# Optimization experiments

Measured on AMD Instinct MI355X. Metric: run time of the kernel, lower is better.

## Reference

```python
import jax, jax.numpy as jnp
import numpy as np

N_HEAD = 16
RMS_EPS = 1.1920928955078125e-07  # torch float32 finfo eps (F.rms_norm default)


def _apply_rotary(x, cos, sin):
    # x: [B,T,H,D], cos/sin: [1,T,1,D/2]
    d = x.shape[-1] // 2
    x1, x2 = x[..., :d], x[..., d:]
    return jnp.concatenate([x1 * cos + x2 * sin, -x1 * sin + x2 * cos], axis=-1)


def _rms_norm(x):
    var = jnp.mean(jnp.square(x), axis=-1, keepdims=True)
    return x * jax.lax.rsqrt(var + RMS_EPS)


def setup_inputs() -> dict:
    key = jax.random.key(0)
    ks = jax.random.split(key, 5)
    B, T, C, H = 2, 2048, 1024, N_HEAD
    D = C // H
    x = jax.random.normal(ks[0], (B, T, C), dtype=jnp.float32)
    cos = jax.random.uniform(ks[1], (1, T, 1, D // 2), dtype=jnp.float32)
    sin = jax.random.uniform(ks[2], (1, T, 1, D // 2), dtype=jnp.float32)
    kv_w = jax.random.normal(ks[3], (C, C), dtype=jnp.float32) * (C ** -0.5)
    proj_w = jax.random.normal(ks[4], (C, C), dtype=jnp.float32) * (C ** -0.5)
    return {"x": x, "cos": cos, "sin": sin, "kv_w": kv_w, "proj_w": proj_w, "window_left": 1024}


def reference(x, cos, sin, kv_w, proj_w, window_left):
    B, T, C = x.shape
    H = N_HEAD
    D = C // H
    scale = D ** -0.5

    q = x.reshape(B, T, H, D)                       # no Q projection
    kv = (x @ kv_w.T).reshape(B, T, H, D)           # tied K=V projection

    q = _rms_norm(_apply_rotary(q, cos, sin))
    kv = _rms_norm(_apply_rotary(kv, cos, sin))

    # scores: [B,H,T,T]
    scores = jnp.einsum('bqhd,bkhd->bhqk', q, kv) * scale

    pos = jnp.arange(T)
    dist = pos[:, None] - pos[None, :]              # query_pos - key_pos
    allowed = (dist >= 0) & (dist <= window_left)   # causal + sliding window
    scores = jnp.where(allowed[None, None], scores, -jnp.inf)

    attn = jax.nn.softmax(scores, axis=-1)
    out = jnp.einsum('bhqk,bkhd->bqhd', attn, kv).reshape(B, T, C)
    return out @ proj_w.T
```

## Files before the change

kernel.cpp:

```cpp
#include <hip/hip_runtime.h>
#include <hip/hip_bf16.h>

using u16 = unsigned short;
typedef __attribute__((ext_vector_type(8))) short short8v;
typedef __attribute__((ext_vector_type(4))) float f32x4;

#define MFMA16(a, b, c) __builtin_amdgcn_mfma_f32_16x16x32_bf16((a), (b), (c), 0, 0, 0)

#define GLOAD16(g, l) __builtin_amdgcn_global_load_lds(                       \
    (const __attribute__((address_space(1))) void*)(const void*)(g),          \
    (__attribute__((address_space(3))) void*)(void*)(l), 16, 0, 0)

static __device__ __forceinline__ u16 f2bf(float x) {
  __hip_bfloat16 h = __float2bfloat16(x);
  return __builtin_bit_cast(u16, h);
}

__global__ __launch_bounds__(256) void cast_f32_bf16(const float* __restrict__ s,
                                                     u16* __restrict__ d, int n) {
  int i = (blockIdx.x * 256 + threadIdx.x) * 4;
  if (i >= n) return;
  float4 v = *reinterpret_cast<const float4*>(s + i);
  ushort4 o;
  o.x = f2bf(v.x); o.y = f2bf(v.y); o.z = f2bf(v.z); o.w = f2bf(v.w);
  *reinterpret_cast<ushort4*>(d + i) = o;
}

__global__ __launch_bounds__(256) void gemm_bt(const u16* __restrict__ A,
                                               const u16* __restrict__ Bt,
                                               float* __restrict__ C,
                                               int M, int N, int K) {
  __shared__ u16 As[64 * 32];
  __shared__ u16 Bs[128 * 32];
  int bm = blockIdx.x, bn = blockIdx.y;
  int tid = threadIdx.x;
  int wid = tid >> 6, l = tid & 63, lr = l & 15, lg = l >> 4;
  int wr = wid >> 1, wc = wid & 1;

  int srow = l >> 2, scol = (l & 3) * 8;
  const u16* Ag  = A  + (size_t)(bm * 64 + wid * 16 + srow) * K + scol;
  const u16* Bg0 = Bt + (size_t)(bn * 128 + wid * 32 + srow) * K + scol;
  const u16* Bg1 = Bg0 + (size_t)16 * K;
  u16* Asb  = &As[wid * 512];
  u16* Bsb0 = &Bs[wid * 1024];
  u16* Bsb1 = &Bs[wid * 1024 + 512];

  f32x4 acc[2][4];
#pragma unroll
  for (int m = 0; m < 2; m++)
#pragma unroll
    for (int n = 0; n < 4; n++) acc[m][n] = (f32x4){0.f, 0.f, 0.f, 0.f};

  for (int k0 = 0; k0 < K; k0 += 32) {
    __syncthreads();
    GLOAD16(Ag + k0, Asb);
    GLOAD16(Bg0 + k0, Bsb0);
    GLOAD16(Bg1 + k0, Bsb1);
    __syncthreads();

    short8v af[2], bfr[4];
#pragma unroll
    for (int m = 0; m < 2; m++)
      af[m] = *reinterpret_cast<const short8v*>(&As[(wr * 32 + m * 16 + lr) * 32 + lg * 8]);
#pragma unroll
    for (int n = 0; n < 4; n++)
      bfr[n] = *reinterpret_cast<const short8v*>(&Bs[(wc * 64 + n * 16 + lr) * 32 + lg * 8]);
#pragma unroll
    for (int m = 0; m < 2; m++)
#pragma unroll
      for (int n = 0; n < 4; n++) acc[m][n] = MFMA16(af[m], bfr[n], acc[m][n]);
  }

#pragma unroll
  for (int m = 0; m < 2; m++)
#pragma unroll
    for (int n = 0; n < 4; n++)
#pragma unroll
      for (int r = 0; r < 4; r++) {
        int row = bm * 64 + wr * 32 + m * 16 + lg * 4 + r;
        int col = bn * 128 + wc * 64 + n * 16 + lr;
        C[(size_t)row * N + col] = acc[m][n][r];
      }
}

__global__ __launch_bounds__(256) void rope_rms(const float* __restrict__ src,
                                                u16* __restrict__ dst,
                                                const float* __restrict__ cosp,
                                                const float* __restrict__ sinp,
                                                float scale) {
  int R = blockIdx.x * 4 + (threadIdx.x >> 6);
  int l = threadIdx.x & 63;
  int h = R & 15;
  int bt = R >> 4;
  int t = bt & 2047, b = bt >> 11;

  float v = src[((size_t)R << 6) + l];
  float p = __shfl_xor(v, 32);
  float c = cosp[(t << 5) + (l & 31)];
  float s = sinp[(t << 5) + (l & 31)];
  float r = v * c + ((l < 32) ? p * s : -p * s);
  float sq = r * r;
  sq += __shfl_xor(sq, 32);
  sq += __shfl_xor(sq, 16);
  sq += __shfl_xor(sq, 8);
  sq += __shfl_xor(sq, 4);
  sq += __shfl_xor(sq, 2);
  sq += __shfl_xor(sq, 1);
  float inv = rsqrtf(sq * (1.0f / 64.0f) + 1.1920928955078125e-07f) * scale;
  dst[((((size_t)b * 16 + h) * 2048 + t) << 6) + l] = f2bf(r * inv);
}

__global__ __launch_bounds__(256) void transpose_td(const u16* __restrict__ src,
                                                    u16* __restrict__ dst) {
  __shared__ u16 Ld[64][72];
  int t0 = blockIdx.x << 6, bh = blockIdx.y;
  int tid = threadIdx.x;
#pragma unroll
  for (int i = 0; i < 2; i++) {
    int c = tid + i * 256, tr = c >> 3, sg = c & 7;
    *reinterpret_cast<short8v*>(&Ld[tr][sg * 8]) =
        *reinterpret_cast<const short8v*>(src + ((size_t)bh * 2048 + t0 + tr) * 64 + sg * 8);
  }
  __syncthreads();
#pragma unroll
  for (int i = 0; i < 2; i++) {
    int c = tid + i * 256, dr = c >> 3, sg = c & 7;
    short8v v;
#pragma unroll
    for (int j = 0; j < 8; j++) v[j] = (short)Ld[sg * 8 + j][dr];
    *reinterpret_cast<short8v*>(dst + ((size_t)bh * 64 + dr) * 2048 + t0 + sg * 8) = v;
  }
}

__global__ __launch_bounds__(256) void attn_swa(const u16* __restrict__ Q,
                                                const u16* __restrict__ KV,
                                                const u16* __restrict__ KVt,
                                                u16* __restrict__ O,
                                                const int* __restrict__ winp) {
  const int T = 2048;
  int bid = blockIdx.x;
  int bh = bid & 31;
  int qi = 31 - (bid >> 5);
  int q0 = qi << 6;
  int b = bh >> 4, h = bh & 15;
  int W = *winp;
  int tid = threadIdx.x;
  int wid = tid >> 6, l = tid & 63, lr = l & 15, lg = l >> 4;

  __shared__ u16 Kl[64][72];
  __shared__ u16 Vt[64][72];
  __shared__ u16 Pl[4][16][72];

  const u16* Qb = Q + (((size_t)bh * T + q0 + wid * 16 + lr) << 6);
  short8v aq0 = *reinterpret_cast<const short8v*>(Qb + lg * 8);
  short8v aq1 = *reinterpret_cast<const short8v*>(Qb + 32 + lg * 8);

  const short one_bf = (short)0x3F80;
  short8v vones = {one_bf, one_bf, one_bf, one_bf, one_bf, one_bf, one_bf, one_bf};

  float m_run[4], l_run[4];
  f32x4 oacc[4];
#pragma unroll
  for (int r = 0; r < 4; r++) { m_run[r] = -1e30f; l_run[r] = 0.f; }
#pragma unroll
  for (int dt = 0; dt < 4; dt++) oacc[dt] = (f32x4){0.f, 0.f, 0.f, 0.f};

  int lo = q0 - W;
  if (lo < 0) lo = 0;
  lo &= ~63;

  const u16* KVbh  = KV + (((size_t)bh * T) << 6);
  const u16* KVtbh = KVt + ((size_t)bh << 6) * T;
  int r8 = tid >> 3, sg = tid & 7;

  short8v vK0 = *reinterpret_cast<const short8v*>(KVbh + ((size_t)(lo + r8) << 6) + sg * 8);
  short8v vK1 = *reinterpret_cast<const short8v*>(KVbh + ((size_t)(lo + r8 + 32) << 6) + sg * 8);
  short8v vV0 = *reinterpret_cast<const short8v*>(KVtbh + (size_t)r8 * T + lo + sg * 8);
  short8v vV1 = *reinterpret_cast<const short8v*>(KVtbh + (size_t)(r8 + 32) * T + lo + sg * 8);

  for (int kt = lo; kt <= q0; kt += 64) {
    __syncthreads();
    *reinterpret_cast<short8v*>(&Kl[r8][sg * 8]) = vK0;
    *reinterpret_cast<short8v*>(&Kl[r8 + 32][sg * 8]) = vK1;
    *reinterpret_cast<short8v*>(&Vt[r8][sg * 8]) = vV0;
    *reinterpret_cast<short8v*>(&Vt[r8 + 32][sg * 8]) = vV1;
    __syncthreads();
    if (kt < q0) {
      vK0 = *reinterpret_cast<const short8v*>(KVbh + ((size_t)(kt + 64 + r8) << 6) + sg * 8);
      vK1 = *reinterpret_cast<const short8v*>(KVbh + ((size_t)(kt + 64 + r8 + 32) << 6) + sg * 8);
      vV0 = *reinterpret_cast<const short8v*>(KVtbh + (size_t)r8 * T + kt + 64 + sg * 8);
      vV1 = *reinterpret_cast<const short8v*>(KVtbh + (size_t)(r8 + 32) * T + kt + 64 + sg * 8);
    }

    f32x4 s[4];
#pragma unroll
    for (int nt = 0; nt < 4; nt++) {
      s[nt] = (f32x4){0.f, 0.f, 0.f, 0.f};
      short8v b0 = *reinterpret_cast<const short8v*>(&Kl[nt * 16 + lr][lg * 8]);
      s[nt] = MFMA16(aq0, b0, s[nt]);
      short8v b1 = *reinterpret_cast<const short8v*>(&Kl[nt * 16 + lr][32 + lg * 8]);
      s[nt] = MFMA16(aq1, b1, s[nt]);
    }

    bool edge = (kt + 63 > q0 + wid * 16) || ((q0 - kt) + wid * 16 + 15 > W);

    float al4[4];
#pragma unroll
    for (int r = 0; r < 4; r++) {
      float sv[4], mt;
      if (edge) {
        int t = q0 + wid * 16 + lg * 4 + r;
        mt = -3e38f;
#pragma unroll
        for (int nt = 0; nt < 4; nt++) {
          int k = kt + nt * 16 + lr;
          float val = ((k <= t) && (t - k <= W)) ? s[nt][r] : -3e38f;
          sv[nt] = val;
          mt = fmaxf(mt, val);
        }
      } else {
#pragma unroll
        for (int nt = 0; nt < 4; nt++) sv[nt] = s[nt][r];
        mt = fmaxf(fmaxf(sv[0], sv[1]), fmaxf(sv[2], sv[3]));
      }
      mt = fmaxf(mt, __shfl_xor(mt, 1));
      mt = fmaxf(mt, __shfl_xor(mt, 2));
      mt = fmaxf(mt, __shfl_xor(mt, 4));
      mt = fmaxf(mt, __shfl_xor(mt, 8));
      float mn = fmaxf(m_run[r], mt);
      float al = exp2f(m_run[r] - mn);
      m_run[r] = mn;
      al4[r] = al;
#pragma unroll
      for (int nt = 0; nt < 4; nt++) {
        Pl[wid][lg * 4 + r][nt * 16 + lr] = f2bf(exp2f(sv[nt] - mn));
      }
#pragma unroll
      for (int dt = 0; dt < 4; dt++) oacc[dt][r] *= al;
    }

    short8v ap0 = *reinterpret_cast<const short8v*>(&Pl[wid][lr][lg * 8]);
    short8v ap1 = *reinterpret_cast<const short8v*>(&Pl[wid][lr][32 + lg * 8]);
    f32x4 psum = (f32x4){0.f, 0.f, 0.f, 0.f};
    psum = MFMA16(ap0, vones, psum);
    psum = MFMA16(ap1, vones, psum);
#pragma unroll
    for (int dt = 0; dt < 4; dt++) {
      short8v v0 = *reinterpret_cast<const short8v*>(&Vt[dt * 16 + lr][lg * 8]);
      oacc[dt] = MFMA16(ap0, v0, oacc[dt]);
      short8v v1 = *reinterpret_cast<const short8v*>(&Vt[dt * 16 + lr][32 + lg * 8]);
      oacc[dt] = MFMA16(ap1, v1, oacc[dt]);
    }
#pragma unroll
    for (int r = 0; r < 4; r++) l_run[r] = l_run[r] * al4[r] + psum[r];
  }

#pragma unroll
  for (int r = 0; r < 4; r++) {
    int t = q0 + wid * 16 + lg * 4 + r;
    float inv = 1.f / l_run[r];
#pragma unroll
    for (int dt = 0; dt < 4; dt++) {
      O[(((size_t)b * T + t) << 10) + (h << 6) + dt * 16 + lr] = f2bf(oacc[dt][r] * inv);
    }
  }
}

extern "C" void kernel_launch(void* const* d_in, const int* in_sizes, int n_in,
                              void* d_out, int out_size, void* d_ws, size_t ws_size,
                              hipStream_t stream) {
  (void)in_sizes; (void)n_in; (void)out_size; (void)ws_size;
  const float* x    = (const float*)d_in[0];
  const float* cosp = (const float*)d_in[1];
  const float* sinp = (const float*)d_in[2];
  const float* kvw  = (const float*)d_in[3];
  const float* pw   = (const float*)d_in[4];
  const int*   win  = (const int*)d_in[5];

  char* w = (char*)d_ws;
  u16*   xbf   = (u16*)(w);
  u16*   kvwbf = (u16*)(w + (8u << 20));
  u16*   pwbf  = (u16*)(w + (10u << 20));
  float* kvf   = (float*)(w + (12u << 20));
  u16*   kvt   = (u16*)(w + (12u << 20));
  u16*   aout  = (u16*)(w + (20u << 20));
  u16*   kvbf  = (u16*)(w + (28u << 20));
  u16*   qbf   = xbf;

  cast_f32_bf16<<<4096, 256, 0, stream>>>(x, xbf, 4194304);
  cast_f32_bf16<<<1024, 256, 0, stream>>>(kvw, kvwbf, 1048576);
  cast_f32_bf16<<<1024, 256, 0, stream>>>(pw, pwbf, 1048576);

  gemm_bt<<<dim3(64, 8), 256, 0, stream>>>(xbf, kvwbf, kvf, 4096, 1024, 1024);

  rope_rms<<<16384, 256, 0, stream>>>(x, qbf, cosp, sinp, 0.18033688011112042f);
  rope_rms<<<16384, 256, 0, stream>>>(kvf, kvbf, cosp, sinp, 1.0f);

  transpose_td<<<dim3(32, 32), 256, 0, stream>>>(kvbf, kvt);

  attn_swa<<<1024, 256, 0, stream>>>(qbf, kvbf, kvt, aout, win);

  gemm_bt<<<dim3(64, 8), 256, 0, stream>>>(aout, pwbf, (float*)d_out, 4096, 1024, 1024);
}
```

Measured before the change: 203.9 us.

## Double-buffer GEMM LDS tiles and swizzle workgroup order

The bf16 GEMM now ping-pongs between two LDS buffers. It issues the global-to-LDS loads for the next K slice before running the MFMAs on the current one, and uses one barrier per iteration instead of two. It also remaps the block index with an XCD-style swizzle so neighbouring tiles share cache on the same die. The cost is doubled shared memory per block. Correctness also depends on the single barrier covering the async LDS load completion, which relies on an implicit vmcnt wait at the barrier.

New measurement: 199.5 us. -2.2%, faster.

```diff
diff --git a/kernel.cpp b/kernel.cpp
--- a/kernel.cpp
+++ b/kernel.cpp
@@ -30,9 +30,12 @@
                                                const u16* __restrict__ Bt,
                                                float* __restrict__ C,
                                                int M, int N, int K) {
-  __shared__ u16 As[64 * 32];
-  __shared__ u16 Bs[128 * 32];
-  int bm = blockIdx.x, bn = blockIdx.y;
+  __shared__ u16 As[2][64 * 32];
+  __shared__ u16 Bs[2][128 * 32];
+  unsigned flat = blockIdx.y * gridDim.x + blockIdx.x;
+  unsigned nwg = gridDim.x * gridDim.y;
+  unsigned swz = (flat & 7) * (nwg >> 3) + (flat >> 3);
+  int bm = swz % gridDim.x, bn = swz / gridDim.x;
   int tid = threadIdx.x;
   int wid = tid >> 6, l = tid & 63, lr = l & 15, lg = l >> 4;
   int wr = wid >> 1, wc = wid & 1;
@@ -41,9 +44,6 @@
   const u16* Ag  = A  + (size_t)(bm * 64 + wid * 16 + srow) * K + scol;
   const u16* Bg0 = Bt + (size_t)(bn * 128 + wid * 32 + srow) * K + scol;
   const u16* Bg1 = Bg0 + (size_t)16 * K;
-  u16* Asb  = &As[wid * 512];
-  u16* Bsb0 = &Bs[wid * 1024];
-  u16* Bsb1 = &Bs[wid * 1024 + 512];
 
   f32x4 acc[2][4];
 #pragma unroll
@@ -51,24 +51,34 @@
 #pragma unroll
     for (int n = 0; n < 4; n++) acc[m][n] = (f32x4){0.f, 0.f, 0.f, 0.f};
 
+  GLOAD16(Ag, &As[0][wid * 512]);
+  GLOAD16(Bg0, &Bs[0][wid * 1024]);
+  GLOAD16(Bg1, &Bs[0][wid * 1024 + 512]);
+  __syncthreads();
+
+  int cur = 0;
   for (int k0 = 0; k0 < K; k0 += 32) {
+    if (k0 + 32 < K) {
+      int nb = cur ^ 1;
+      GLOAD16(Ag + k0 + 32, &As[nb][wid * 512]);
+      GLOAD16(Bg0 + k0 + 32, &Bs[nb][wid * 1024]);
+      GLOAD16(Bg1 + k0 + 32, &Bs[nb][wid * 1024 + 512]);
+    }
+
+    short8v af[2], bfr[4];
+#pragma unroll
+    for (int m = 0; m < 2; m++)
+      af[m] = *reinterpret_cast<const short8v*>(&As[cur][(wr * 32 + m * 16 + lr) * 32 + lg * 8]);
+#pragma unroll
+    for (int n = 0; n < 4; n++)
+      bfr[n] = *reinterpret_cast<const short8v*>(&Bs[cur][(wc * 64 + n * 16 + lr) * 32 + lg * 8]);
+#pragma unroll
+    for (int m = 0; m < 2; m++)
+#pragma unroll
+      for (int n = 0; n < 4; n++) acc[m][n] = MFMA16(af[m], bfr[n], acc[m][n]);
+
     __syncthreads();
-    GLOAD16(Ag + k0, Asb);
-    GLOAD16(Bg0 + k0, Bsb0);
-    GLOAD16(Bg1 + k0, Bsb1);
-    __syncthreads();
-
-    short8v af[2], bfr[4];
-#pragma unroll
-    for (int m = 0; m < 2; m++)
-      af[m] = *reinterpret_cast<const short8v*>(&As[(wr * 32 + m * 16 + lr) * 32 + lg * 8]);
-#pragma unroll
-    for (int n = 0; n < 4; n++)
-      bfr[n] = *reinterpret_cast<const short8v*>(&Bs[(wc * 64 + n * 16 + lr) * 32 + lg * 8]);
-#pragma unroll
-    for (int m = 0; m < 2; m++)
-#pragma unroll
-      for (int n = 0; n < 4; n++) acc[m][n] = MFMA16(af[m], bfr[n], acc[m][n]);
+    cur ^= 1;
   }
 
 #pragma unroll
```
